# Kernel optimization log

Hardware: AMD Instinct MI355X
Metric: run time of the kernel (lower is better)

Reference implementation:

```python
import jax, jax.numpy as jnp
import numpy as np

N = 8192  # number of DAG nodes


def setup_inputs() -> dict:
    key = jax.random.key(0)
    k1, k2, k3 = jax.random.split(key, 3)
    thresholds = jax.random.normal(k1, (N,), dtype=jnp.float32)
    # children in [-1, N): -1 marks a leaf (no child)
    left = jax.random.randint(k2, (N,), -1, N, dtype=jnp.int32)
    right = jax.random.randint(k3, (N,), -1, N, dtype=jnp.int32)
    return {"thresholds": thresholds, "left": left, "right": right}


def reference(thresholds, left, right):
    # BFS fixed-point reachability from node 0, N sequential relaxation steps.
    n_nodes = left.shape[0]

    def step(reachable, _):
        # route children of reachable non-leaf nodes into a scatter; dump
        # inactive slots into the sentinel index n_nodes (dropped on slice)
        active_left = jnp.where(reachable & (left >= 0), left, n_nodes)
        active_right = jnp.where(reachable & (right >= 0), right, n_nodes)
        new_reachable = jnp.zeros(n_nodes + 1, dtype=jnp.bool_)
        new_reachable = new_reachable.at[active_left].set(True)
        new_reachable = new_reachable.at[active_right].set(True)
        new_reachable = new_reachable.at[0].set(True)
        return (new_reachable[:n_nodes] | reachable, None)

    init = jnp.zeros(n_nodes, dtype=jnp.bool_).at[0].set(True)
    mask, _ = jax.lax.scan(step, init, None, length=n_nodes)
    return mask
```

## Files before the change

### kernel.cpp

```cpp
#include <hip/hip_runtime.h>


#define NMAX   8192
#define BLK    1024
#define NWORDS (NMAX / 32)
#define INNER  4

__global__ __launch_bounds__(BLK) void dag_reach_kernel(
    const int* __restrict__ left,
    const int* __restrict__ right,
    int* __restrict__ out,
    int n)
{
    __shared__ int2 sLR[NMAX];
    __shared__ unsigned int reach[NWORDS];
    __shared__ int s_flag[3];

    const int tid = threadIdx.x;

    {
        const int i = 8 * tid;
        if (i + 7 < n) {
            int4 l0 = *reinterpret_cast<const int4*>(left  + i);
            int4 l1 = *reinterpret_cast<const int4*>(left  + i + 4);
            int4 r0 = *reinterpret_cast<const int4*>(right + i);
            int4 r1 = *reinterpret_cast<const int4*>(right + i + 4);
            sLR[i + 0] = make_int2(l0.x, r0.x);
            sLR[i + 1] = make_int2(l0.y, r0.y);
            sLR[i + 2] = make_int2(l0.z, r0.z);
            sLR[i + 3] = make_int2(l0.w, r0.w);
            sLR[i + 4] = make_int2(l1.x, r1.x);
            sLR[i + 5] = make_int2(l1.y, r1.y);
            sLR[i + 6] = make_int2(l1.z, r1.z);
            sLR[i + 7] = make_int2(l1.w, r1.w);
        } else {
            for (int k = i; k < n; ++k) sLR[k] = make_int2(left[k], right[k]);
        }
    }
    if (tid < NWORDS) reach[tid] = (tid == 0) ? 1u : 0u;
    if (tid < 3)      s_flag[tid] = 0;
    __syncthreads();

    const int word_idx = tid >> 2;
    const int shift    = (tid & 3) * 8;
    const int base     = tid * 8;
    unsigned int expanded = 0u;
    volatile unsigned int* vreach = reach;

    int p3 = 0;
    while (true) {
        const int pn3 = (p3 == 2) ? 0 : p3 + 1;
        int ch = 0;

        #pragma unroll
        for (int it = 0; it < INNER; ++it) {
            unsigned int pend = ((vreach[word_idx] >> shift) & 0xFFu) & ~expanded;
            if (pend) {
                ch = 1;
                expanded |= pend;
                while (pend) {
                    int b0 = __ffs(pend) - 1; pend &= pend - 1;
                    int b1 = -1, b2 = -1, b3 = -1;
                    if (pend) { b1 = __ffs(pend) - 1; pend &= pend - 1;
                        if (pend) { b2 = __ffs(pend) - 1; pend &= pend - 1;
                            if (pend) { b3 = __ffs(pend) - 1; pend &= pend - 1; } } }
                    int2 e0 = sLR[base + b0];
                    int2 e1 = sLR[base + (b1 < 0 ? b0 : b1)];
                    int2 e2 = sLR[base + (b2 < 0 ? b0 : b2)];
                    int2 e3 = sLR[base + (b3 < 0 ? b0 : b3)];
                    if (e0.x >= 0) atomicOr(&reach[e0.x >> 5], 1u << (e0.x & 31));
                    if (e0.y >= 0) atomicOr(&reach[e0.y >> 5], 1u << (e0.y & 31));
                    if (b1 >= 0) {
                        if (e1.x >= 0) atomicOr(&reach[e1.x >> 5], 1u << (e1.x & 31));
                        if (e1.y >= 0) atomicOr(&reach[e1.y >> 5], 1u << (e1.y & 31));
                    }
                    if (b2 >= 0) {
                        if (e2.x >= 0) atomicOr(&reach[e2.x >> 5], 1u << (e2.x & 31));
                        if (e2.y >= 0) atomicOr(&reach[e2.y >> 5], 1u << (e2.y & 31));
                    }
                    if (b3 >= 0) {
                        if (e3.x >= 0) atomicOr(&reach[e3.x >> 5], 1u << (e3.x & 31));
                        if (e3.y >= 0) atomicOr(&reach[e3.y >> 5], 1u << (e3.y & 31));
                    }
                }
            }
        }

        if ((tid & 63) == 0) s_flag[pn3] = 0;
        if (__any(ch) && (tid & 63) == 0) s_flag[p3] = 1;
        __syncthreads();
        if (!s_flag[p3]) break;
        p3 = pn3;
    }

    for (int i = 4 * tid; i < n; i += 4 * BLK) {
        const unsigned w = reach[i >> 5];
        const int b = i & 31;
        *reinterpret_cast<int4*>(out + i) =
            make_int4((int)((w >> (b + 0)) & 1u),
                      (int)((w >> (b + 1)) & 1u),
                      (int)((w >> (b + 2)) & 1u),
                      (int)((w >> (b + 3)) & 1u));
    }
}

extern "C" void kernel_launch(void* const* d_in, const int* in_sizes, int n_in,
                              void* d_out, int out_size, void* d_ws, size_t ws_size,
                              hipStream_t stream)
{
    const int* left  = (const int*)d_in[1];
    const int* right = (const int*)d_in[2];
    int* out = (int*)d_out;
    const int n = in_sizes[1];

    dag_reach_kernel<<<1, BLK, 0, stream>>>(left, right, out, n);
}
```

Before: 74.33 us.

## Precompute depth-3 descendant lists to cut BFS barrier rounds

Each node's grandchildren-of-grandchildren (up to 8 nodes at depth 3) are precomputed and packed as 16-bit indices into shared memory, so every expansion step jumps three levels at once. Node 0's first two descendant levels are seeded directly into the reachable set, and the inner iteration count drops from 4 to 2. The aim is fewer block-wide barrier rounds in the fixed-point loop, which is latency-bound on one workgroup. In exchange there is a precompute phase of dependent shared-memory gathers, more atomics per expanded node, and a 128KB shared array that assumes 16-bit node indices.

```diff
diff --git a/kernel.cpp b/kernel.cpp
--- a/kernel.cpp
+++ b/kernel.cpp
@@ -4,7 +4,7 @@
 #define NMAX   8192
 #define BLK    1024
 #define NWORDS (NMAX / 32)
-#define INNER  4
+#define SENT   0xFFFFu
 
 __global__ __launch_bounds__(BLK) void dag_reach_kernel(
     const int* __restrict__ left,
@@ -12,40 +12,90 @@
     int* __restrict__ out,
     int n)
 {
-    __shared__ int2 sLR[NMAX];
+    __shared__ __align__(16) unsigned short A3[NMAX * 8];
     __shared__ unsigned int reach[NWORDS];
     __shared__ int s_flag[3];
 
-    const int tid = threadIdx.x;
+    int2* A2 = reinterpret_cast<int2*>(A3);
 
-    {
-        const int i = 8 * tid;
-        if (i + 7 < n) {
-            int4 l0 = *reinterpret_cast<const int4*>(left  + i);
-            int4 l1 = *reinterpret_cast<const int4*>(left  + i + 4);
-            int4 r0 = *reinterpret_cast<const int4*>(right + i);
-            int4 r1 = *reinterpret_cast<const int4*>(right + i + 4);
-            sLR[i + 0] = make_int2(l0.x, r0.x);
-            sLR[i + 1] = make_int2(l0.y, r0.y);
-            sLR[i + 2] = make_int2(l0.z, r0.z);
-            sLR[i + 3] = make_int2(l0.w, r0.w);
-            sLR[i + 4] = make_int2(l1.x, r1.x);
-            sLR[i + 5] = make_int2(l1.y, r1.y);
-            sLR[i + 6] = make_int2(l1.z, r1.z);
-            sLR[i + 7] = make_int2(l1.w, r1.w);
-        } else {
-            for (int k = i; k < n; ++k) sLR[k] = make_int2(left[k], right[k]);
+    const int tid  = threadIdx.x;
+    const int base = tid * 8;
+
+    if (base + 7 < n) {
+        int4 l0 = *reinterpret_cast<const int4*>(left  + base);
+        int4 l1 = *reinterpret_cast<const int4*>(left  + base + 4);
+        int4 r0 = *reinterpret_cast<const int4*>(right + base);
+        int4 r1 = *reinterpret_cast<const int4*>(right + base + 4);
+        A2[base + 0] = make_int2(l0.x, r0.x);
+        A2[base + 1] = make_int2(l0.y, r0.y);
+        A2[base + 2] = make_int2(l0.z, r0.z);
+        A2[base + 3] = make_int2(l0.w, r0.w);
+        A2[base + 4] = make_int2(l1.x, r1.x);
+        A2[base + 5] = make_int2(l1.y, r1.y);
+        A2[base + 6] = make_int2(l1.z, r1.z);
+        A2[base + 7] = make_int2(l1.w, r1.w);
+    } else {
+        for (int k = base; k < n; ++k) A2[k] = make_int2(left[k], right[k]);
+    }
+    if (tid < NWORDS) reach[tid] = 0u;
+    if (tid < 3)      s_flag[tid] = 0;
+    __syncthreads();
+
+    int4 h[8];
+    #pragma unroll
+    for (int j = 0; j < 8; ++j) {
+        const int v = base + j;
+        const int SS = (int)(SENT | (SENT << 16));
+        int4 w = make_int4(SS, SS, SS, SS);
+        if (v < n) {
+            int2 c  = A2[v];
+            int2 g0 = (c.x  >= 0) ? A2[c.x]  : make_int2(-1, -1);
+            int2 g1 = (c.y  >= 0) ? A2[c.y]  : make_int2(-1, -1);
+            int2 q0 = (g0.x >= 0) ? A2[g0.x] : make_int2(-1, -1);
+            int2 q1 = (g0.y >= 0) ? A2[g0.y] : make_int2(-1, -1);
+            int2 q2 = (g1.x >= 0) ? A2[g1.x] : make_int2(-1, -1);
+            int2 q3 = (g1.y >= 0) ? A2[g1.y] : make_int2(-1, -1);
+            #define PK(a, b) (int)(((a) >= 0 ? (unsigned)(a) : SENT) | \
+                                   (((b) >= 0 ? (unsigned)(b) : SENT) << 16))
+            w = make_int4(PK(q0.x, q0.y), PK(q1.x, q1.y),
+                          PK(q2.x, q2.y), PK(q3.x, q3.y));
+            #undef PK
+            if (v == 0) {
+                atomicOr(&reach[0], 1u);
+                if (c.x  >= 0) atomicOr(&reach[c.x  >> 5], 1u << (c.x  & 31));
+                if (c.y  >= 0) atomicOr(&reach[c.y  >> 5], 1u << (c.y  & 31));
+                if (g0.x >= 0) atomicOr(&reach[g0.x >> 5], 1u << (g0.x & 31));
+                if (g0.y >= 0) atomicOr(&reach[g0.y >> 5], 1u << (g0.y & 31));
+                if (g1.x >= 0) atomicOr(&reach[g1.x >> 5], 1u << (g1.x & 31));
+                if (g1.y >= 0) atomicOr(&reach[g1.y >> 5], 1u << (g1.y & 31));
+            }
         }
+        h[j] = w;
     }
-    if (tid < NWORDS) reach[tid] = (tid == 0) ? 1u : 0u;
-    if (tid < 3)      s_flag[tid] = 0;
+    __syncthreads();
+
+    #pragma unroll
+    for (int j = 0; j < 8; ++j) {
+        *reinterpret_cast<int4*>(&A3[(base + j) * 8]) = h[j];
+    }
     __syncthreads();
 
     const int word_idx = tid >> 2;
     const int shift    = (tid & 3) * 8;
-    const int base     = tid * 8;
     unsigned int expanded = 0u;
     volatile unsigned int* vreach = reach;
+
+    #define EXPAND8(W) do {                                                   \
+        unsigned _a;                                                          \
+        _a = (unsigned)(W).x & 0xFFFFu; if (_a != SENT) atomicOr(&reach[_a >> 5], 1u << (_a & 31)); \
+        _a = (unsigned)(W).x >> 16;     if (_a != SENT) atomicOr(&reach[_a >> 5], 1u << (_a & 31)); \
+        _a = (unsigned)(W).y & 0xFFFFu; if (_a != SENT) atomicOr(&reach[_a >> 5], 1u << (_a & 31)); \
+        _a = (unsigned)(W).y >> 16;     if (_a != SENT) atomicOr(&reach[_a >> 5], 1u << (_a & 31)); \
+        _a = (unsigned)(W).z & 0xFFFFu; if (_a != SENT) atomicOr(&reach[_a >> 5], 1u << (_a & 31)); \
+        _a = (unsigned)(W).z >> 16;     if (_a != SENT) atomicOr(&reach[_a >> 5], 1u << (_a & 31)); \
+        _a = (unsigned)(W).w & 0xFFFFu; if (_a != SENT) atomicOr(&reach[_a >> 5], 1u << (_a & 31)); \
+        _a = (unsigned)(W).w >> 16;     if (_a != SENT) atomicOr(&reach[_a >> 5], 1u << (_a & 31)); \
+    } while (0)
 
     int p3 = 0;
     while (true) {
@@ -53,35 +103,20 @@
         int ch = 0;
 
         #pragma unroll
-        for (int it = 0; it < INNER; ++it) {
+        for (int it = 0; it < 2; ++it) {
             unsigned int pend = ((vreach[word_idx] >> shift) & 0xFFu) & ~expanded;
             if (pend) {
                 ch = 1;
                 expanded |= pend;
                 while (pend) {
                     int b0 = __ffs(pend) - 1; pend &= pend - 1;
-                    int b1 = -1, b2 = -1, b3 = -1;
-                    if (pend) { b1 = __ffs(pend) - 1; pend &= pend - 1;
-                        if (pend) { b2 = __ffs(pend) - 1; pend &= pend - 1;
-                            if (pend) { b3 = __ffs(pend) - 1; pend &= pend - 1; } } }
-                    int2 e0 = sLR[base + b0];
-                    int2 e1 = sLR[base + (b1 < 0 ? b0 : b1)];
-                    int2 e2 = sLR[base + (b2 < 0 ? b0 : b2)];
-                    int2 e3 = sLR[base + (b3 < 0 ? b0 : b3)];
-                    if (e0.x >= 0) atomicOr(&reach[e0.x >> 5], 1u << (e0.x & 31));
-                    if (e0.y >= 0) atomicOr(&reach[e0.y >> 5], 1u << (e0.y & 31));
-                    if (b1 >= 0) {
-                        if (e1.x >= 0) atomicOr(&reach[e1.x >> 5], 1u << (e1.x & 31));
-                        if (e1.y >= 0) atomicOr(&reach[e1.y >> 5], 1u << (e1.y & 31));
-                    }
-                    if (b2 >= 0) {
-                        if (e2.x >= 0) atomicOr(&reach[e2.x >> 5], 1u << (e2.x & 31));
-                        if (e2.y >= 0) atomicOr(&reach[e2.y >> 5], 1u << (e2.y & 31));
-                    }
-                    if (b3 >= 0) {
-                        if (e3.x >= 0) atomicOr(&reach[e3.x >> 5], 1u << (e3.x & 31));
-                        if (e3.y >= 0) atomicOr(&reach[e3.y >> 5], 1u << (e3.y & 31));
-                    }
+                    int b1 = -1;
+                    if (pend) { b1 = __ffs(pend) - 1; pend &= pend - 1; }
+                    int4 w0 = *reinterpret_cast<const int4*>(&A3[(base + b0) * 8]);
+                    int4 w1 = *reinterpret_cast<const int4*>(
+                                  &A3[(base + (b1 < 0 ? b0 : b1)) * 8]);
+                    EXPAND8(w0);
+                    if (b1 >= 0) EXPAND8(w1);
                 }
             }
         }
@@ -92,6 +127,7 @@
         if (!s_flag[p3]) break;
         p3 = pn3;
     }
+    #undef EXPAND8
 
     for (int i = 4 * tid; i < n; i += 4 * BLK) {
         const unsigned w = reach[i >> 5];
```

Measured after the change: 78.51 us. 5.6% more time.
